# Kernel tuning notes

Hardware: AMD Instinct MI355X
Metric: run time of the kernel (lower is better)

## Reference

```python
import jax, jax.numpy as jnp
import numpy as np

VNUM = 50000
D = 256
NE = 1600000


def setup_inputs() -> dict:
    key = jax.random.key(0)
    ks = jax.random.split(key, 10)
    return {
        "vrepr": jax.random.normal(ks[0], (VNUM, D), dtype=jnp.float32) * 0.1,
        "sidx": jax.random.randint(ks[1], (NE,), 0, VNUM, dtype=jnp.int32),
        "tidx": jax.random.randint(ks[2], (NE,), 0, VNUM, dtype=jnp.int32),
        "esgn": jnp.where(jax.random.uniform(ks[3], (NE,)) < 0.5, -1.0, 1.0).astype(jnp.float32),
        "enorm": jax.random.uniform(ks[4], (NE,), dtype=jnp.float32),
        "loc_w": jax.random.normal(ks[5], (D, D), dtype=jnp.float32) / np.sqrt(D),
        "loc_b": jax.random.normal(ks[6], (D,), dtype=jnp.float32) * 0.01,
        "std_w": jax.random.normal(ks[7], (D, D), dtype=jnp.float32) / np.sqrt(D),
        "std_b": jax.random.normal(ks[8], (D,), dtype=jnp.float32) * 0.01,
        "eps": jax.random.normal(ks[9], (VNUM, D), dtype=jnp.float32),
    }


def reference(vrepr, sidx, tidx, esgn, enorm, loc_w, loc_b, std_w, std_b, eps):
    # GraphConv: gather source node features, weight by enorm*esgn, scatter-add to targets
    w = (enorm * esgn)[:, None]              # [E, 1]
    msg = vrepr[sidx] * w                    # [E, D]
    ptr = jax.ops.segment_sum(msg, tidx, num_segments=vrepr.shape[0])  # [V, D]
    # Linear heads (torch Linear: y = x @ W.T + b)
    loc = ptr @ loc_w.T + loc_b
    std = jax.nn.softplus(ptr @ std_w.T + std_b) + 1e-7
    # rsample: loc + std * eps
    vsample = loc + std * eps
    return loc, std, vsample
```

## Files before the change

### kernel.cpp

```cpp
#include <hip/hip_runtime.h>

#define D 256

typedef __attribute__((ext_vector_type(8))) short s16x8;
typedef __attribute__((ext_vector_type(4))) float f32x4;

static __device__ __forceinline__ unsigned short f2b(float f) {
    unsigned u = __float_as_uint(f);
    unsigned r = (u + 0x7fffu + ((u >> 16) & 1u)) >> 16;
    return (unsigned short)r;
}
static __device__ __forceinline__ unsigned pack2(float a, float b) {
    return (unsigned)f2b(a) | ((unsigned)f2b(b) << 16);
}

static __device__ __forceinline__ void gload_lds16(const void* g, void* l) {
    __builtin_amdgcn_global_load_lds((const __attribute__((address_space(1))) unsigned int*)g,
                                     (__attribute__((address_space(3))) unsigned int*)l,
                                     16, 0, 0);
}

__global__ void prep_w_kernel(const float* __restrict__ lw, const float* __restrict__ sw,
                              unsigned short* __restrict__ wTf) {
    int i = blockIdx.x * 256 + threadIdx.x;
    float v = (i < D * D) ? lw[i] : sw[i - D * D];
    int n = i >> 8;
    int k = i & 255;
    int lane = (n & 15) | (((k >> 3) & 3) << 4);
    int unit = ((n >> 4) << 9) + ((k >> 5) << 6) + lane;
    wTf[unit * 8 + (k & 7)] = f2b(v);
}

__global__ void conv_v_kernel(const float* __restrict__ vr, unsigned short* __restrict__ vb, int n8) {
    int i = blockIdx.x * 256 + threadIdx.x;
    if (i < n8) {
        float4 f0 = ((const float4*)vr)[2 * i];
        float4 f1 = ((const float4*)vr)[2 * i + 1];
        uint4 o;
        o.x = pack2(f0.x, f0.y);
        o.y = pack2(f0.z, f0.w);
        o.z = pack2(f1.x, f1.y);
        o.w = pack2(f1.z, f1.w);
        ((uint4*)vb)[i] = o;
    }
}

__global__ void hist_kernel(const int* __restrict__ tidx, int* __restrict__ cnt,
                            int* __restrict__ rank, int E) {
    int e = blockIdx.x * blockDim.x + threadIdx.x;
    if (e < E) rank[e] = atomicAdd(&cnt[tidx[e]], 1);
}

__global__ void scan1_kernel(const int* __restrict__ cnt, int* __restrict__ bsum, int V) {
    __shared__ int red[256];
    int b = blockIdx.x, tid = threadIdx.x;
    int base = b * 1024 + tid * 4;
    int s = 0;
    if (base + 3 < V) {
        int4 q = *(const int4*)&cnt[base];
        s = q.x + q.y + q.z + q.w;
    } else {
        for (int j = 0; j < 4; ++j)
            if (base + j < V) s += cnt[base + j];
    }
    red[tid] = s;
    __syncthreads();
    for (int ofs = 128; ofs > 0; ofs >>= 1) {
        if (tid < ofs) red[tid] += red[tid + ofs];
        __syncthreads();
    }
    if (tid == 0) bsum[b] = red[0];
}

__global__ void scan2_kernel(int* __restrict__ bsum, int nb) {
    __shared__ int s[256];
    int tid = threadIdx.x;
    int v = (tid < nb) ? bsum[tid] : 0;
    s[tid] = v;
    __syncthreads();
    for (int ofs = 1; ofs < 256; ofs <<= 1) {
        int t = (tid >= ofs) ? s[tid - ofs] : 0;
        __syncthreads();
        s[tid] += t;
        __syncthreads();
    }
    if (tid < nb) bsum[tid] = s[tid] - v;
}

__global__ void scan3_kernel(const int* __restrict__ cnt, const int* __restrict__ bsum,
                             int* __restrict__ off, int V, int E) {
    __shared__ int ts[256];
    int b = blockIdx.x, tid = threadIdx.x;
    int base = b * 1024 + tid * 4;
    int v0 = 0, v1 = 0, v2 = 0, v3 = 0;
    if (base + 3 < V) {
        int4 q = *(const int4*)&cnt[base];
        v0 = q.x; v1 = q.y; v2 = q.z; v3 = q.w;
    } else {
        if (base < V)     v0 = cnt[base];
        if (base + 1 < V) v1 = cnt[base + 1];
        if (base + 2 < V) v2 = cnt[base + 2];
        if (base + 3 < V) v3 = cnt[base + 3];
    }
    int tsum = v0 + v1 + v2 + v3;
    ts[tid] = tsum;
    __syncthreads();
    for (int ofs = 1; ofs < 256; ofs <<= 1) {
        int t = (tid >= ofs) ? ts[tid - ofs] : 0;
        __syncthreads();
        ts[tid] += t;
        __syncthreads();
    }
    int pre = bsum[b] + ts[tid] - tsum;
    if (base + 3 < V) {
        int4 o = make_int4(pre, pre + v0, pre + v0 + v1, pre + v0 + v1 + v2);
        *(int4*)&off[base] = o;
    } else {
        if (base < V)     off[base] = pre;
        if (base + 1 < V) off[base + 1] = pre + v0;
        if (base + 2 < V) off[base + 2] = pre + v0 + v1;
        if (base + 3 < V) off[base + 3] = pre + v0 + v1 + v2;
    }
    if (b == 0 && tid == 0) off[V] = E;
}

__global__ void fill_kernel(const int* __restrict__ sidx, const int* __restrict__ tidx,
                            const float* __restrict__ esgn, const float* __restrict__ enorm,
                            const int* __restrict__ off, const int* __restrict__ rank,
                            int2* __restrict__ pk, int E) {
    int e = blockIdx.x * blockDim.x + threadIdx.x;
    if (e >= E) return;
    int idx = off[tidx[e]] + rank[e];
    float w = enorm[e] * esgn[e];
    pk[idx] = make_int2(sidx[e], __float_as_int(w));
}

#define FMA8(A, W)                                                   \
    acc[0] = fmaf(__uint_as_float((A).x << 16), (W), acc[0]);        \
    acc[1] = fmaf(__uint_as_float((A).x & 0xffff0000u), (W), acc[1]);\
    acc[2] = fmaf(__uint_as_float((A).y << 16), (W), acc[2]);        \
    acc[3] = fmaf(__uint_as_float((A).y & 0xffff0000u), (W), acc[3]);\
    acc[4] = fmaf(__uint_as_float((A).z << 16), (W), acc[4]);        \
    acc[5] = fmaf(__uint_as_float((A).z & 0xffff0000u), (W), acc[5]);\
    acc[6] = fmaf(__uint_as_float((A).w << 16), (W), acc[6]);        \
    acc[7] = fmaf(__uint_as_float((A).w & 0xffff0000u), (W), acc[7]);

__global__ __launch_bounds__(256) void accum_kernel(const unsigned short* __restrict__ vb,
                                                    const int2* __restrict__ pk,
                                                    const int* __restrict__ off,
                                                    unsigned short* __restrict__ ptrf, int V) {
    int gid = blockIdx.x * blockDim.x + threadIdx.x;
    int v = gid >> 6;
    if (v >= V) return;
    int lane = threadIdx.x & 63;
    int half = lane >> 5;
    int c = lane & 31;
    int beg = off[v], end = off[v + 1];
    int mid = beg + ((end - beg + 1) >> 1);
    int i = half ? mid : beg;
    int e = half ? end : mid;
    const uint4* base = (const uint4*)vb;
    float acc[8];
#pragma unroll
    for (int j = 0; j < 8; ++j) acc[j] = 0.f;
    for (; i + 3 < e; i += 4) {
        int2 p0 = pk[i];
        int2 p1 = pk[i + 1];
        int2 p2 = pk[i + 2];
        int2 p3 = pk[i + 3];
        uint4 a0 = base[(size_t)p0.x * 32 + c];
        uint4 a1 = base[(size_t)p1.x * 32 + c];
        uint4 a2 = base[(size_t)p2.x * 32 + c];
        uint4 a3 = base[(size_t)p3.x * 32 + c];
        float w0 = __int_as_float(p0.y);
        float w1 = __int_as_float(p1.y);
        float w2 = __int_as_float(p2.y);
        float w3 = __int_as_float(p3.y);
        FMA8(a0, w0)
        FMA8(a1, w1)
        FMA8(a2, w2)
        FMA8(a3, w3)
    }
    for (; i < e; ++i) {
        int2 p = pk[i];
        float w = __int_as_float(p.y);
        uint4 a = base[(size_t)p.x * 32 + c];
        FMA8(a, w)
    }
#pragma unroll
    for (int j = 0; j < 8; ++j) acc[j] += __shfl_xor(acc[j], 32, 64);
    if (half == 0) {
        uint4 o;
        o.x = pack2(acc[0], acc[1]);
        o.y = pack2(acc[2], acc[3]);
        o.z = pack2(acc[4], acc[5]);
        o.w = pack2(acc[6], acc[7]);
        int fl = (v & 15) | ((c & 3) << 4);
        int unit = ((v >> 4) << 9) + ((c >> 2) << 6) + fl;
        ((uint4*)ptrf)[unit] = o;
    }
}

__global__ __launch_bounds__(256, 4) void head_mfma_kernel(const unsigned short* __restrict__ ptrf,
                                                           const unsigned short* __restrict__ wTf,
                                                           const float* __restrict__ lb,
                                                           const float* __restrict__ sb,
                                                           const float* __restrict__ eps,
                                                           float* __restrict__ out, int V) {
    __shared__ s16x8 Blds[2][1024];
    int tid = threadIdx.x;
    int wave = tid >> 6, lane = tid & 63;
    int nhalf = blockIdx.x;
    int nb = nhalf << 3;
    int mt = blockIdx.y * 4 + wave;
    int lastmt = (V - 1) >> 4;
    int mtc = mt > lastmt ? lastmt : mt;
    int v0 = mt << 4;

    const s16x8* Af = (const s16x8*)ptrf + ((size_t)mtc << 9) + lane;
    s16x8 a[8];
#pragma unroll
    for (int kt = 0; kt < 8; ++kt) a[kt] = Af[kt << 6];

    const s16x8* Bf = (const s16x8*)wTf;

    f32x4 acc[16];
    f32x4 zero = {0.f, 0.f, 0.f, 0.f};
#pragma unroll
    for (int nt = 0; nt < 16; ++nt) acc[nt] = zero;

#define STAGE_B(KT, BUF)                                                      \
    {                                                                         \
        _Pragma("unroll")                                                     \
        for (int j = 0; j < 4; ++j) {                                         \
            int ln = j * 4 + wave;                                            \
            int nt = (ln < 8) ? (nb + ln) : (16 + nb + (ln - 8));             \
            gload_lds16((const void*)(Bf + (nt << 9) + ((KT) << 6) + lane),   \
                        (void*)&Blds[BUF][ln << 6]);                          \
        }                                                                     \
    }

    STAGE_B(0, 0);
    __syncthreads();

#pragma unroll
    for (int kt = 0; kt < 8; ++kt) {
        int buf = kt & 1;
        if (kt < 7) STAGE_B(kt + 1, buf ^ 1);
#pragma unroll
        for (int ln = 0; ln < 16; ++ln) {
            s16x8 b = Blds[buf][(ln << 6) + lane];
            acc[ln] = __builtin_amdgcn_mfma_f32_16x16x32_bf16(a[kt], b, acc[ln], 0, 0, 0);
        }
        if (kt < 7) __syncthreads();
    }
#undef STAGE_B

    if (v0 < V) {
        int quad = lane >> 4, m16 = lane & 15;
        size_t VD = (size_t)V * D;
        const float* epsb = eps + (size_t)v0 * D;
        float* outb = out + (size_t)v0 * D;
#pragma unroll
        for (int ln = 0; ln < 8; ++ln) {
            int col = (nhalf << 7) + (ln << 4) + m16;
            float lbv = lb[col];
            float sbv = sb[col];
#pragma unroll
            for (int r = 0; r < 4; ++r) {
                int row = (quad << 2) + r;
                int o = row * D + col;
                float lo = acc[ln][r] + lbv;
                float pre = acc[ln + 8][r] + sbv;
                float sp = fmaxf(pre, 0.f) + __logf(1.f + __expf(-fabsf(pre)));
                float st = sp + 1e-7f;
                float ep = __builtin_nontemporal_load(&epsb[o]);
                outb[o] = lo;
                outb[VD + o] = st;
                outb[2 * VD + o] = fmaf(st, ep, lo);
            }
        }
    }
}

extern "C" void kernel_launch(void* const* d_in, const int* in_sizes, int n_in,
                              void* d_out, int out_size, void* d_ws, size_t ws_size,
                              hipStream_t stream) {
    const float* vrepr = (const float*)d_in[0];
    const int*   sidx  = (const int*)d_in[1];
    const int*   tidx  = (const int*)d_in[2];
    const float* esgn  = (const float*)d_in[3];
    const float* enorm = (const float*)d_in[4];
    const float* loc_w = (const float*)d_in[5];
    const float* loc_b = (const float*)d_in[6];
    const float* std_w = (const float*)d_in[7];
    const float* std_b = (const float*)d_in[8];
    const float* eps   = (const float*)d_in[9];
    float* out = (float*)d_out;

    int E = in_sizes[1];
    int V = in_sizes[0] / D;

    char* ws = (char*)d_ws;
    size_t o = 0;
    unsigned short* vb   = (unsigned short*)(ws + o); o += (size_t)V * D * 2;
    unsigned short* ptrf = (unsigned short*)(ws + o); o += (size_t)V * D * 2;
    unsigned short* wTf  = (unsigned short*)(ws + o); o += (size_t)2 * D * D * 2;
    int* off  = (int*)(ws + o); o += ((size_t)V + 16) * sizeof(int);
    int* cnt  = (int*)(ws + o); o += ((size_t)V + 16) * sizeof(int);
    int* rank = (int*)(ws + o); o += (size_t)E * sizeof(int);
    int* bsum = (int*)(ws + o); o += 256 * sizeof(int);
    o = (o + 15) & ~(size_t)15;
    int2* pk = (int2*)(ws + o); o += (size_t)E * sizeof(int2);

    int nb = (V + 1023) >> 10;

    hipMemsetAsync(cnt, 0, (size_t)V * sizeof(int), stream);
    prep_w_kernel<<<(2 * D * D) / 256, 256, 0, stream>>>(loc_w, std_w, wTf);
    conv_v_kernel<<<(V * (D / 8) + 255) / 256, 256, 0, stream>>>(vrepr, vb, V * (D / 8));
    hist_kernel<<<(E + 255) / 256, 256, 0, stream>>>(tidx, cnt, rank, E);
    scan1_kernel<<<nb, 256, 0, stream>>>(cnt, bsum, V);
    scan2_kernel<<<1, 256, 0, stream>>>(bsum, nb);
    scan3_kernel<<<nb, 256, 0, stream>>>(cnt, bsum, off, V, E);
    fill_kernel<<<(E + 255) / 256, 256, 0, stream>>>(sidx, tidx, esgn, enorm, off, rank, pk, E);
    accum_kernel<<<(V * 64 + 255) / 256, 256, 0, stream>>>(vb, pk, off, ptrf, V);
    dim3 hgrid(2, (V + 63) / 64);
    head_mfma_kernel<<<hgrid, 256, 0, stream>>>(ptrf, wTf, loc_b, std_b, eps, out, V);
}
```

Measured before the change: 525.2 us.

## Fuse prep kernels, drop rank buffer via atomic cursors, merge scan stages

Three setup launches (cnt memset, weight bf16 packing, vrepr conversion) become one multi-role kernel, and the weight packing is vectorized to float4 loads. The per-edge rank array is removed: the histogram atomics no longer return values, and the fill kernel claims slots with atomics on a cursor array that the scan seeds with the exclusive offsets. The single-block scan2 is folded into scan3, where each block sums the preceding block totals itself. The aim is fewer launches and less per-edge memory traffic, at the cost of a second atomic pass in fill and a nondeterministic edge order within each segment, which changes float summation order.

```diff
diff --git a/kernel.cpp b/kernel.cpp
--- a/kernel.cpp
+++ b/kernel.cpp
@@ -20,35 +20,54 @@
                                      16, 0, 0);
 }
 
-__global__ void prep_w_kernel(const float* __restrict__ lw, const float* __restrict__ sw,
-                              unsigned short* __restrict__ wTf) {
-    int i = blockIdx.x * 256 + threadIdx.x;
-    float v = (i < D * D) ? lw[i] : sw[i - D * D];
-    int n = i >> 8;
-    int k = i & 255;
-    int lane = (n & 15) | (((k >> 3) & 3) << 4);
-    int unit = ((n >> 4) << 9) + ((k >> 5) << 6) + lane;
-    wTf[unit * 8 + (k & 7)] = f2b(v);
-}
-
-__global__ void conv_v_kernel(const float* __restrict__ vr, unsigned short* __restrict__ vb, int n8) {
-    int i = blockIdx.x * 256 + threadIdx.x;
-    if (i < n8) {
-        float4 f0 = ((const float4*)vr)[2 * i];
-        float4 f1 = ((const float4*)vr)[2 * i + 1];
-        uint4 o;
-        o.x = pack2(f0.x, f0.y);
-        o.y = pack2(f0.z, f0.w);
-        o.z = pack2(f1.x, f1.y);
-        o.w = pack2(f1.z, f1.w);
-        ((uint4*)vb)[i] = o;
-    }
-}
-
-__global__ void hist_kernel(const int* __restrict__ tidx, int* __restrict__ cnt,
-                            int* __restrict__ rank, int E) {
+__global__ void prep_conv_kernel(const float* __restrict__ vr,
+                                 const float* __restrict__ lw, const float* __restrict__ sw,
+                                 unsigned short* __restrict__ vb,
+                                 unsigned short* __restrict__ wTf,
+                                 int* __restrict__ cnt,
+                                 int n8, int nvb, int nwb, int ncnt) {
+    int b = blockIdx.x;
+    if (b < nvb) {
+        int i = b * 256 + threadIdx.x;
+        if (i < n8) {
+            float4 f0 = ((const float4*)vr)[2 * i];
+            float4 f1 = ((const float4*)vr)[2 * i + 1];
+            uint4 o;
+            o.x = pack2(f0.x, f0.y);
+            o.y = pack2(f0.z, f0.w);
+            o.z = pack2(f1.x, f1.y);
+            o.w = pack2(f1.z, f1.w);
+            ((uint4*)vb)[i] = o;
+        }
+    } else if (b < nvb + nwb) {
+        int i = (b - nvb) * 256 + threadIdx.x;
+        int e0 = i * 4;
+        if (e0 < 2 * D * D) {
+            const float* src = (e0 < D * D) ? (lw + e0) : (sw + (e0 - D * D));
+            float4 f = *(const float4*)src;
+            int n = e0 >> 8;
+            int k0 = e0 & 255;
+            int lane = (n & 15) | (((k0 >> 3) & 3) << 4);
+            int unit = ((n >> 4) << 9) + ((k0 >> 5) << 6) + lane;
+            uint2 o;
+            o.x = pack2(f.x, f.y);
+            o.y = pack2(f.z, f.w);
+            *(uint2*)&wTf[unit * 8 + (k0 & 7)] = o;
+        }
+    } else {
+        int i = ((b - nvb - nwb) * 256 + threadIdx.x) * 4;
+        if (i + 3 < ncnt) {
+            *(int4*)&cnt[i] = make_int4(0, 0, 0, 0);
+        } else {
+            for (int j = 0; j < 4; ++j)
+                if (i + j < ncnt) cnt[i + j] = 0;
+        }
+    }
+}
+
+__global__ void hist_kernel(const int* __restrict__ tidx, int* __restrict__ cnt, int E) {
     int e = blockIdx.x * blockDim.x + threadIdx.x;
-    if (e < E) rank[e] = atomicAdd(&cnt[tidx[e]], 1);
+    if (e < E) atomicAdd(&cnt[tidx[e]], 1);
 }
 
 __global__ void scan1_kernel(const int* __restrict__ cnt, int* __restrict__ bsum, int V) {
@@ -72,25 +91,18 @@
     if (tid == 0) bsum[b] = red[0];
 }
 
-__global__ void scan2_kernel(int* __restrict__ bsum, int nb) {
-    __shared__ int s[256];
-    int tid = threadIdx.x;
-    int v = (tid < nb) ? bsum[tid] : 0;
-    s[tid] = v;
-    __syncthreads();
-    for (int ofs = 1; ofs < 256; ofs <<= 1) {
-        int t = (tid >= ofs) ? s[tid - ofs] : 0;
-        __syncthreads();
-        s[tid] += t;
-        __syncthreads();
-    }
-    if (tid < nb) bsum[tid] = s[tid] - v;
-}
-
-__global__ void scan3_kernel(const int* __restrict__ cnt, const int* __restrict__ bsum,
-                             int* __restrict__ off, int V, int E) {
+__global__ void scan3_kernel(int* __restrict__ cnt, const int* __restrict__ bsum,
+                             int* __restrict__ off, int V, int E, int nb) {
     __shared__ int ts[256];
+    __shared__ int pref;
     int b = blockIdx.x, tid = threadIdx.x;
+    if (tid < 64) {
+        int val = 0;
+        for (int c = tid; c < b; c += 64) val += bsum[c];
+#pragma unroll
+        for (int ofs = 32; ofs > 0; ofs >>= 1) val += __shfl_xor(val, ofs, 64);
+        if (tid == 0) pref = val;
+    }
     int base = b * 1024 + tid * 4;
     int v0 = 0, v1 = 0, v2 = 0, v3 = 0;
     if (base + 3 < V) {
@@ -111,26 +123,26 @@
         ts[tid] += t;
         __syncthreads();
     }
-    int pre = bsum[b] + ts[tid] - tsum;
+    int pre = pref + ts[tid] - tsum;
     if (base + 3 < V) {
         int4 o = make_int4(pre, pre + v0, pre + v0 + v1, pre + v0 + v1 + v2);
         *(int4*)&off[base] = o;
+        *(int4*)&cnt[base] = o;
     } else {
-        if (base < V)     off[base] = pre;
-        if (base + 1 < V) off[base + 1] = pre + v0;
-        if (base + 2 < V) off[base + 2] = pre + v0 + v1;
-        if (base + 3 < V) off[base + 3] = pre + v0 + v1 + v2;
+        if (base < V)     { off[base] = pre;                cnt[base] = pre; }
+        if (base + 1 < V) { off[base + 1] = pre + v0;       cnt[base + 1] = pre + v0; }
+        if (base + 2 < V) { off[base + 2] = pre + v0 + v1;  cnt[base + 2] = pre + v0 + v1; }
+        if (base + 3 < V) { off[base + 3] = pre + v0 + v1 + v2; cnt[base + 3] = pre + v0 + v1 + v2; }
     }
     if (b == 0 && tid == 0) off[V] = E;
 }
 
 __global__ void fill_kernel(const int* __restrict__ sidx, const int* __restrict__ tidx,
                             const float* __restrict__ esgn, const float* __restrict__ enorm,
-                            const int* __restrict__ off, const int* __restrict__ rank,
-                            int2* __restrict__ pk, int E) {
+                            int* __restrict__ cur, int2* __restrict__ pk, int E) {
     int e = blockIdx.x * blockDim.x + threadIdx.x;
     if (e >= E) return;
-    int idx = off[tidx[e]] + rank[e];
+    int idx = atomicAdd(&cur[tidx[e]], 1);
     float w = enorm[e] * esgn[e];
     pk[idx] = make_int2(sidx[e], __float_as_int(w));
 }
@@ -290,6 +302,7 @@
     const int*   sidx  = (const int*)d_in[1];
     const int*   tidx  = (const int*)d_in[2];
     const float* esgn  = (const float*)d_in[3];
+    const float* esgn4 = esgn;
     const float* enorm = (const float*)d_in[4];
     const float* loc_w = (const float*)d_in[5];
     const float* loc_b = (const float*)d_in[6];
@@ -297,6 +310,7 @@
     const float* std_b = (const float*)d_in[8];
     const float* eps   = (const float*)d_in[9];
     float* out = (float*)d_out;
+    (void)esgn4;
 
     int E = in_sizes[1];
     int V = in_sizes[0] / D;
@@ -308,21 +322,23 @@
     unsigned short* wTf  = (unsigned short*)(ws + o); o += (size_t)2 * D * D * 2;
     int* off  = (int*)(ws + o); o += ((size_t)V + 16) * sizeof(int);
     int* cnt  = (int*)(ws + o); o += ((size_t)V + 16) * sizeof(int);
-    int* rank = (int*)(ws + o); o += (size_t)E * sizeof(int);
     int* bsum = (int*)(ws + o); o += 256 * sizeof(int);
     o = (o + 15) & ~(size_t)15;
     int2* pk = (int2*)(ws + o); o += (size_t)E * sizeof(int2);
 
     int nb = (V + 1023) >> 10;
-
-    hipMemsetAsync(cnt, 0, (size_t)V * sizeof(int), stream);
-    prep_w_kernel<<<(2 * D * D) / 256, 256, 0, stream>>>(loc_w, std_w, wTf);
-    conv_v_kernel<<<(V * (D / 8) + 255) / 256, 256, 0, stream>>>(vrepr, vb, V * (D / 8));
-    hist_kernel<<<(E + 255) / 256, 256, 0, stream>>>(tidx, cnt, rank, E);
+    int n8 = V * (D / 8);
+    int nvb = (n8 + 255) / 256;
+    int nwb = (2 * D * D + 1023) / 1024;
+    int ncnt = V + 16;
+    int ncb = (ncnt + 1023) / 1024;
+
+    prep_conv_kernel<<<nvb + nwb + ncb, 256, 0, stream>>>(vrepr, loc_w, std_w, vb, wTf, cnt,
+                                                          n8, nvb, nwb, ncnt);
+    hist_kernel<<<(E + 255) / 256, 256, 0, stream>>>(tidx, cnt, E);
     scan1_kernel<<<nb, 256, 0, stream>>>(cnt, bsum, V);
-    scan2_kernel<<<1, 256, 0, stream>>>(bsum, nb);
-    scan3_kernel<<<nb, 256, 0, stream>>>(cnt, bsum, off, V, E);
-    fill_kernel<<<(E + 255) / 256, 256, 0, stream>>>(sidx, tidx, esgn, enorm, off, rank, pk, E);
+    scan3_kernel<<<nb, 256, 0, stream>>>(cnt, bsum, off, V, E, nb);
+    fill_kernel<<<(E + 255) / 256, 256, 0, stream>>>(sidx, tidx, esgn, enorm, cnt, pk, E);
     accum_kernel<<<(V * 64 + 255) / 256, 256, 0, stream>>>(vb, pk, off, ptrf, V);
     dim3 hgrid(2, (V + 63) / 64);
     head_mfma_kernel<<<hgrid, 256, 0, stream>>>(ptrf, wTf, loc_b, std_b, eps, out, V);
```

Measured after the change: 582.7 us. 11.0% more time.
